# Performance work log

Hardware: AMD Instinct MI355X
Metric: run time of the kernel (lower is better)

Reference implementation:

```python
import jax, jax.numpy as jnp
import numpy as np
import math

B, C, H, W = 8, 64, 256, 256
E, NH = 256, 8
HD = E // NH  # 32


def get_coords(h, w):
    xx, yy = jnp.meshgrid(jnp.arange(h, dtype=jnp.float32), jnp.arange(w, dtype=jnp.float32), indexing='ij')
    return jnp.stack((xx.reshape(-1), yy.reshape(-1)), axis=-1)  # [N, 2]


def setup_inputs() -> dict:
    key = jax.random.key(0)
    ks = jax.random.split(key, 12)
    def xavier(k, shape):
        fan_out, fan_in = shape
        a = math.sqrt(6.0 / (fan_in + fan_out))
        return jax.random.uniform(k, shape, jnp.float32, -a, a)
    x = jax.random.normal(ks[0], (B, C, H, W), jnp.float32)
    z = jax.random.normal(ks[1], (B, C), jnp.float32)
    pos = jax.random.uniform(ks[2], (B, NH, 2), jnp.float32) * (H - 1)
    Wq = xavier(ks[3], (E, C)); bq = jnp.zeros((E,), jnp.float32)
    Wk = xavier(ks[4], (E, C)); bk = jnp.zeros((E,), jnp.float32)
    Wv = xavier(ks[5], (E, C)); bv = jnp.zeros((E,), jnp.float32)
    Wp = xavier(ks[6], (HD, 2)); bp = jax.random.uniform(ks[7], (HD,), jnp.float32, -1.0, 1.0) / math.sqrt(2.0)
    return {"x": x, "z": z, "pos": pos, "Wq": Wq, "bq": bq, "Wk": Wk, "bk": bk,
            "Wv": Wv, "bv": bv, "Wp": Wp, "bp": bp}


def reference(x, z, pos, Wq, bq, Wk, bk, Wv, bv, Wp, bp):
    b, c, h, w = x.shape
    n = h * w
    x_flat = x.reshape(b, c, n).transpose(0, 2, 1)          # [B, N, C]
    pos_grid = get_coords(h, w)                              # [N, 2]
    q = (z @ Wq.T + bq).reshape(b, NH, HD)                   # [B, H, hd]
    k = (x_flat @ Wk.T + bk).reshape(b, n, NH, HD)           # [B, N, H, hd]
    # relative-position modulation of keys
    rel = pos_grid[None, :, None, :] - pos[:, None, :, :]    # [B, N, H, 2]
    qxk = rel @ Wp.T + bp                                    # [B, N, H, hd]
    k = k * qxk
    v = x_flat @ Wv.T + bv                                   # [B, N, E]
    attn_logits = jnp.einsum('bhc,bnhc->bnh', q, k) / math.sqrt(HD)
    attention = jax.nn.softmax(attn_logits, axis=1)          # softmax over N
    pos_out = jnp.einsum('bnh,nx->bhx', attention, pos_grid) # [B, H, 2]
    values = jnp.einsum('bnh,bnc->bhc', attention, v)        # [B, H, E]
    return (values, pos_out)
```

## Files before the change

kernel.cpp:

```cpp
#include <hip/hip_runtime.h>

#define NN    65536
#define NSUB  128
#define NBLK  (NN/NSUB)
#define NTILE 8

typedef short bf16x8 __attribute__((ext_vector_type(8)));
typedef float f32x4v __attribute__((ext_vector_type(4)));
typedef unsigned short ushort_t;
typedef unsigned int uint_t;

#define BUFSZ   36864
#define XLO_OFF 18432
#define SLICE   4608
#define LGSTR   28
#define PSTR    40
#define PST_OFF 1536
#define RED_B   73728
#define SMEM_BYTES 74112

#define WTHI_B  0
#define WTLO_B  32768
#define CJ_B    65536
#define PM_B    66304
#define PL_B    197376
#define PSP_B   328448
#define PSX_B   590592
#define Q_B     8979200
#define QSTR    68

__device__ __forceinline__ uint_t bf16_rne_bits(float f) {
  uint_t u = __float_as_uint(f);
  return (u + 0x7FFFu + ((u >> 16) & 1u)) >> 16;
}
__device__ __forceinline__ uint_t cvt_pk_bf16(float a, float b) {
  uint_t r;
  asm("v_cvt_pk_bf16_f32 %0, %1, %2" : "=v"(r) : "v"(a), "v"(b));
  return r;
}
template <int CTRL, int RMASK = 0xf>
__device__ __forceinline__ float dpp_add(float x) {
  int t = __builtin_amdgcn_update_dpp(0, __float_as_int(x), CTRL, RMASK, 0xf, false);
  return x + __int_as_float(t);
}
template <int CTRL, int RMASK = 0xf>
__device__ __forceinline__ float dpp_maxs(float x) {
  int t = __builtin_amdgcn_update_dpp((int)0xFF800000u, __float_as_int(x), CTRL, RMASK, 0xf, false);
  return fmaxf(x, __int_as_float(t));
}
__device__ __forceinline__ float half_sum(float x) {
  x = dpp_add<0x111>(x); x = dpp_add<0x112>(x); x = dpp_add<0x114>(x);
  x = dpp_add<0x118>(x); x = dpp_add<0x142, 0xA>(x);
  return x;
}
__device__ __forceinline__ float half_max(float x) {
  x = dpp_maxs<0x111>(x); x = dpp_maxs<0x112>(x); x = dpp_maxs<0x114>(x);
  x = dpp_maxs<0x118>(x); x = dpp_maxs<0x142, 0xA>(x);
  return x;
}

__global__ __launch_bounds__(64) void prep_kernel(
    const float* __restrict__ z,  const float* __restrict__ Wq, const float* __restrict__ bq,
    const float* __restrict__ Wk, const float* __restrict__ bk,
    const float* __restrict__ Wp, const float* __restrict__ bp,
    ushort_t* __restrict__ WThi, ushort_t* __restrict__ WTlo, float* __restrict__ Cj)
{
  const int h = blockIdx.x, b = blockIdx.y, t = threadIdx.x;
  __shared__ float q[32];
  if (t < 32) {
    const int e = h*32 + t;
    float a = bq[e];
    const float* zr = z + b*64;
    const float* wr = Wq + e*64;
    #pragma unroll 8
    for (int c = 0; c < 64; ++c) a += zr[c]*wr[c];
    q[t] = a;
  }
  __syncthreads();
  const int c = t;
  float w[3] = {0.f, 0.f, 0.f};
  #pragma unroll 4
  for (int hd = 0; hd < 32; ++hd) {
    const float qk = q[hd] * Wk[(h*32+hd)*64 + c];
    w[0] += qk * bp[hd];
    w[1] += qk * Wp[hd*2+0];
    w[2] += qk * Wp[hd*2+1];
  }
  #pragma unroll
  for (int j = 0; j < 3; ++j) {
    const int coeff = h*3 + j;
    const uint_t hb = bf16_rne_bits(w[j]);
    const float  fh = __uint_as_float(hb << 16);
    const uint_t lb = bf16_rne_bits(w[j] - fh);
    WThi[(b*32 + coeff)*64 + c] = (ushort_t)hb;
    WTlo[(b*32 + coeff)*64 + c] = (ushort_t)lb;
  }
  if (h == 0) {
    #pragma unroll
    for (int r = 0; r < 8; ++r) {
      WThi[(b*32 + 24 + r)*64 + c] = 0;
      WTlo[(b*32 + 24 + r)*64 + c] = 0;
    }
  }
  if (t < 3) {
    float s = 0.f;
    for (int hd = 0; hd < 32; ++hd) {
      const float m = (t == 0) ? bp[hd] : Wp[hd*2 + (t-1)];
      s += q[hd] * m * bk[h*32+hd];
    }
    Cj[b*24 + h*3 + t] = s;
  }
}

__global__ __launch_bounds__(256, 2) void main_kernel(
    const float* __restrict__ x, const float* __restrict__ pos,
    const ushort_t* __restrict__ WThi, const ushort_t* __restrict__ WTlo,
    const float* __restrict__ Cj,
    float* __restrict__ Pm, float* __restrict__ Pl,
    float* __restrict__ Psp, float* __restrict__ Psx)
{
  extern __shared__ char smc[];
  float* red = (float*)(smc + RED_B);
  const int t    = threadIdx.x;
  const int blk0 = blockIdx.x;
  const int b    = blockIdx.y;
  const int w    = t >> 6, lid = t & 63;
  const int c0   = lid & 15, q4 = lid >> 4;
  const int hg   = lid >> 5, pxl = lid & 31;

  bf16x8 bh[2][2], bl[2][2];
  {
    const ushort_t* wtb_h = WThi + b*2048;
    const ushort_t* wtb_l = WTlo + b*2048;
    #pragma unroll
    for (int nt = 0; nt < 2; ++nt)
      #pragma unroll
      for (int ks = 0; ks < 2; ++ks) {
        const int off = (nt*16 + c0)*64 + ks*32 + q4*8;
        bh[nt][ks] = *(const bf16x8*)(wtb_h + off);
        bl[nt][ks] = *(const bf16x8*)(wtb_l + off);
      }
  }

  float cj[12];
  {
    const float* cjp = Cj + b*24 + hg*12;
    #pragma unroll
    for (int k = 0; k < 12; ++k) cj[k] = cjp[k];
  }
  float posx[4], py[4];
  #pragma unroll
  for (int hl = 0; hl < 4; ++hl) {
    const int h = hg*4 + hl;
    posx[hl] = pos[(b*8+h)*2 + 0];
    py[hl]   = pos[(b*8+h)*2 + 1];
  }

  const int qd  = lid & 7;
  const int g   = lid >> 3;
  const int swz = (4*w + (qd >> 1)) & 7;
  const int chnk = (g ^ swz) * 16;
  const float* xg = x + (size_t)b*64*NN + (size_t)g*8*NN
                      + (size_t)blk0*NTILE*NSUB + w*32 + 4*qd;
  f32x4v v[8];
  #pragma unroll
  for (int j = 0; j < 8; ++j) v[j] = *(const f32x4v*)(xg + (size_t)j*NN);

  for (int it = 0; it < NTILE; ++it) {
    const int blk = blk0*NTILE + it;
    char* bufb  = smc + (it & 1)*BUFSZ;
    char* xhiB  = bufb;
    char* xloB  = bufb + XLO_OFF;
    char* slice = xloB + w*SLICE;

    #pragma unroll
    for (int i = 0; i < 4; ++i) {
      uint_t H[4], L[4];
      #pragma unroll
      for (int jp = 0; jp < 4; ++jp) {
        const float f0 = v[2*jp][i], f1 = v[2*jp+1][i];
        const uint_t hpk = cvt_pk_bf16(f0, f1);
        const float h0 = __uint_as_float(hpk << 16);
        const float h1 = __uint_as_float(hpk & 0xFFFF0000u);
        const uint_t l0 = __float_as_uint(f0 - h0);
        const uint_t l1 = __float_as_uint(f1 - h1);
        H[jp] = hpk;
        L[jp] = __builtin_amdgcn_perm(l1, l0, 0x07060302u);
      }
      const int row = w*32 + 4*qd + i;
      *(uint4*)(xhiB + row*144 + chnk) = make_uint4(H[0], H[1], H[2], H[3]);
      *(uint4*)(xloB + row*144 + chnk) = make_uint4(L[0], L[1], L[2], L[3]);
    }

    if (it + 1 < NTILE) {
      xg += NSUB;
      #pragma unroll
      for (int j = 0; j < 8; ++j) v[j] = *(const f32x4v*)(xg + (size_t)j*NN);
    }

    f32x4v acc[2][2];
    #pragma unroll
    for (int mt = 0; mt < 2; ++mt) { acc[mt][0] = (f32x4v)0.f; acc[mt][1] = (f32x4v)0.f; }
    #pragma unroll
    for (int mt = 0; mt < 2; ++mt) {
      const int row  = w*32 + mt*16 + c0;
      const int srow = (4*w + 2*mt + (c0 >> 3)) & 7;
      const int ch0  = (q4 ^ srow) * 16;
      const char* rh = xhiB + row*144;
      const char* rl = xloB + row*144;
      bf16x8 ah0 = *(const bf16x8*)(rh + ch0);
      bf16x8 ah1 = *(const bf16x8*)(rh + (ch0 ^ 64));
      bf16x8 al0 = *(const bf16x8*)(rl + ch0);
      bf16x8 al1 = *(const bf16x8*)(rl + (ch0 ^ 64));
      #pragma unroll
      for (int nt = 0; nt < 2; ++nt) {
        f32x4v a = acc[mt][nt];
        a = __builtin_amdgcn_mfma_f32_16x16x32_bf16(ah0, bh[nt][0], a, 0, 0, 0);
        a = __builtin_amdgcn_mfma_f32_16x16x32_bf16(ah1, bh[nt][1], a, 0, 0, 0);
        a = __builtin_amdgcn_mfma_f32_16x16x32_bf16(ah0, bl[nt][0], a, 0, 0, 0);
        a = __builtin_amdgcn_mfma_f32_16x16x32_bf16(ah1, bl[nt][1], a, 0, 0, 0);
        a = __builtin_amdgcn_mfma_f32_16x16x32_bf16(al0, bh[nt][0], a, 0, 0, 0);
        a = __builtin_amdgcn_mfma_f32_16x16x32_bf16(al1, bh[nt][1], a, 0, 0, 0);
        acc[mt][nt] = a;
      }
    }

    {
      float* lga_w = (float*)slice;
      #pragma unroll
      for (int mt = 0; mt < 2; ++mt)
        #pragma unroll
        for (int r = 0; r < 4; ++r) {
          const int prow = mt*16 + q4*4 + r;
          lga_w[prow*LGSTR + c0] = acc[mt][0][r];
          if (c0 < 8) lga_w[prow*LGSTR + 16 + c0] = acc[mt][1][r];
        }
    }

    float a12[12];
    {
      const float4* ap = (const float4*)((float*)slice + pxl*LGSTR + hg*12);
      #pragma unroll
      for (int r = 0; r < 3; ++r) *(float4*)(a12 + 4*r) = ap[r];
    }
    const float gxf = (float)(blk >> 1);
    const float tf  = (float)(((blk & 1) << 7) + w*32 + pxl);
    float lg[4];
    #pragma unroll
    for (int hl = 0; hl < 4; ++hl) {
      const float a0 = a12[hl*3+0] + cj[hl*3+0];
      const float a1 = a12[hl*3+1] + cj[hl*3+1];
      const float a2 = a12[hl*3+2] + cj[hl*3+2];
      lg[hl] = (a0 + (gxf - posx[hl])*a1 + (tf - py[hl])*a2) * 0.17677669529663687f;
    }

    #pragma unroll
    for (int hl = 0; hl < 4; ++hl) {
      const float m = half_max(lg[hl]);
      if ((lid & 31) == 31) red[w*8 + hg*4 + hl] = m;
    }
    __syncthreads();

    float p[4];
    #pragma unroll
    for (int hl = 0; hl < 4; ++hl) {
      const int h = hg*4 + hl;
      const float M = fmaxf(fmaxf(red[0*8+h], red[1*8+h]), fmaxf(red[2*8+h], red[3*8+h]));
      p[hl] = __expf(lg[hl] - M);
    }

    #pragma unroll
    for (int hl = 0; hl < 4; ++hl) {
      const float sp  = half_sum(p[hl]);
      const float spj = half_sum(p[hl] * tf);
      if ((lid & 31) == 31) {
        red[32 + w*8 + hg*4 + hl] = sp;
        red[64 + w*8 + hg*4 + hl] = spj;
      }
    }
    {
      ushort_t* pls = (ushort_t*)slice;
      #pragma unroll
      for (int hl = 0; hl < 4; ++hl) {
        const int h = hg*4 + hl;
        const uint_t hb = bf16_rne_bits(p[hl]);
        const float  hf = __uint_as_float(hb << 16);
        const uint_t lb = __float_as_uint(p[hl] - hf) >> 16;
        pls[h*PSTR + pxl]     = (ushort_t)hb;
        pls[(h+8)*PSTR + pxl] = (ushort_t)lb;
      }
    }

    {
      const ushort_t* pls = (const ushort_t*)slice;
      const bf16x8 afr = *(const bf16x8*)(pls + c0*PSTR + q4*8);
      const int srow_b = (4*w + q4) & 7;
      float* pst = (float*)(slice + PST_OFF);
      #pragma unroll
      for (int nt = 0; nt < 4; ++nt) {
        const int gch  = nt*2 + (c0 >> 3);
        const char* base = xhiB + (w*32 + q4*8)*144 + ((gch ^ srow_b)*16) + (c0 & 7)*2;
        bf16x8 bfr;
        #pragma unroll
        for (int j = 0; j < 8; ++j) bfr[j] = *(const short*)(base + j*144);
        f32x4v accB = __builtin_amdgcn_mfma_f32_16x16x32_bf16(afr, bfr, (f32x4v)0.f, 0, 0, 0);
        #pragma unroll
        for (int r = 0; r < 4; ++r) {
          const float o = __shfl_xor(accB[r], 32, 64);
          if (q4 < 2) pst[(q4*4 + r)*64 + nt*16 + c0] = accB[r] + o;
        }
      }
    }
    __syncthreads();

    if (t < 8) {
      const int base = (b*NBLK + blk)*8 + t;
      const float M  = fmaxf(fmaxf(red[0*8+t], red[8+t]), fmaxf(red[16+t], red[24+t]));
      const float L  = red[32+t] + red[40+t] + red[48+t] + red[56+t];
      const float SJ = red[64+t] + red[72+t] + red[80+t] + red[88+t];
      Pm[base] = M;
      Pl[base] = L;
      Psp[base*2+0] = gxf * L;
      Psp[base*2+1] = SJ;
    }
    {
      const size_t pb64 = ((size_t)(b*NBLK + blk))*8*64;
      #pragma unroll
      for (int r = 0; r < 2; ++r) {
        const int idx = t + 256*r;
        float s = 0.f;
        #pragma unroll
        for (int w2 = 0; w2 < 4; ++w2)
          s += *(const float*)(xloB + w2*SLICE + PST_OFF + idx*4);
        Psx[pb64 + idx] = s;
      }
    }
  }
}

__global__ __launch_bounds__(256) void reduce1_kernel(
    const float* __restrict__ Pm, const float* __restrict__ Pl,
    const float* __restrict__ Psp, const float* __restrict__ Psx,
    float* __restrict__ Q)
{
  const int g = blockIdx.x, h = blockIdx.y, b = blockIdx.z, t = threadIdx.x;
  __shared__ float al[64];
  __shared__ float mgs;
  __shared__ float sums[3];
  __shared__ float sxl[256];
  const int base = (b*NBLK + g*64)*8 + h;

  float m_t = -1e30f;
  if (t < 64) {
    m_t = Pm[base + t*8];
    float mm = m_t;
    #pragma unroll
    for (int off = 32; off >= 1; off >>= 1) mm = fmaxf(mm, __shfl_xor(mm, off, 64));
    if (t == 0) mgs = mm;
  }
  __syncthreads();
  const float Mg = mgs;
  if (t < 64) {
    const float a = __expf(m_t - Mg);
    al[t] = a;
    float lt = Pl[base + t*8] * a;
    float sx = Psp[(base + t*8)*2 + 0] * a;
    float sy = Psp[(base + t*8)*2 + 1] * a;
    #pragma unroll
    for (int off = 32; off >= 1; off >>= 1) {
      lt += __shfl_xor(lt, off, 64);
      sx += __shfl_xor(sx, off, 64);
      sy += __shfl_xor(sy, off, 64);
    }
    if (t == 0) { sums[0] = lt; sums[1] = sx; sums[2] = sy; }
  }
  __syncthreads();
  {
    const int c = t & 63, g2 = t >> 6;
    float acc = 0.f;
    #pragma unroll
    for (int i = 0; i < 16; ++i) {
      const int k = g2*16 + i;
      acc += al[k] * Psx[(size_t)(base + k*8)*64 + c];
    }
    sxl[g2*64 + c] = acc;
  }
  __syncthreads();
  float* q = Q + ((b*8 + h)*8 + g)*QSTR;
  if (t < 64) q[4+t] = sxl[t] + sxl[64+t] + sxl[128+t] + sxl[192+t];
  if (t == 0) { q[0] = Mg; q[1] = sums[0]; q[2] = sums[1]; q[3] = sums[2]; }
}

__global__ __launch_bounds__(64) void reduce2_kernel(
    const float* __restrict__ Q, const float* __restrict__ Wv, const float* __restrict__ bv,
    float* __restrict__ out)
{
  const int h = blockIdx.x, b = blockIdx.y, t = threadIdx.x;
  __shared__ float qm[8], bl[8], l8[8], sx8[8], sy8[8];
  __shared__ float SXs[64];
  const float* qb = Q + ((b*8 + h)*8)*QSTR;

  if (t < 8) qm[t] = qb[t*QSTR + 0];
  __syncthreads();
  float M = qm[0];
  #pragma unroll
  for (int g = 1; g < 8; ++g) M = fmaxf(M, qm[g]);
  if (t < 8) {
    const float be = __expf(qm[t] - M);
    bl[t]  = be;
    l8[t]  = be * qb[t*QSTR + 1];
    sx8[t] = be * qb[t*QSTR + 2];
    sy8[t] = be * qb[t*QSTR + 3];
  }
  __syncthreads();
  float L = 0.f;
  #pragma unroll
  for (int g = 0; g < 8; ++g) L += l8[g];
  const float invL = 1.0f / L;
  {
    float s = 0.f;
    #pragma unroll
    for (int g = 0; g < 8; ++g) s += bl[g] * qb[g*QSTR + 4 + t];
    SXs[t] = s * invL;
  }
  __syncthreads();

  #pragma unroll
  for (int r = 0; r < 4; ++r) {
    const int e = t + 64*r;
    float v = bv[e];
    const float* wvr = Wv + e*64;
    #pragma unroll 8
    for (int c = 0; c < 64; ++c) v += wvr[c] * SXs[c];
    out[(b*8 + h)*256 + e] = v;
  }
  if (t == 0) {
    float spx = 0.f, spy = 0.f;
    #pragma unroll
    for (int g = 0; g < 8; ++g) { spx += sx8[g]; spy += sy8[g]; }
    out[16384 + (b*8 + h)*2 + 0] = spx * invL;
    out[16384 + (b*8 + h)*2 + 1] = spy * invL;
  }
}

extern "C" void kernel_launch(void* const* d_in, const int* in_sizes, int n_in,
                              void* d_out, int out_size, void* d_ws, size_t ws_size,
                              hipStream_t stream)
{
  const float* x   = (const float*)d_in[0];
  const float* z   = (const float*)d_in[1];
  const float* pos = (const float*)d_in[2];
  const float* Wq  = (const float*)d_in[3];
  const float* bq  = (const float*)d_in[4];
  const float* Wk  = (const float*)d_in[5];
  const float* bk  = (const float*)d_in[6];
  const float* Wv  = (const float*)d_in[7];
  const float* bv  = (const float*)d_in[8];
  const float* Wp  = (const float*)d_in[9];
  const float* bp  = (const float*)d_in[10];
  float* out = (float*)d_out;
  char*  wsb = (char*)d_ws;

  ushort_t* WThi = (ushort_t*)(wsb + WTHI_B);
  ushort_t* WTlo = (ushort_t*)(wsb + WTLO_B);
  float* Cj  = (float*)(wsb + CJ_B);
  float* Pm  = (float*)(wsb + PM_B);
  float* Pl  = (float*)(wsb + PL_B);
  float* Psp = (float*)(wsb + PSP_B);
  float* Psx = (float*)(wsb + PSX_B);
  float* Q   = (float*)(wsb + Q_B);

  (void)hipFuncSetAttribute((const void*)main_kernel,
                            hipFuncAttributeMaxDynamicSharedMemorySize, SMEM_BYTES);

  prep_kernel   <<<dim3(8,8),          64,  0,          stream>>>(z, Wq, bq, Wk, bk, Wp, bp, WThi, WTlo, Cj);
  main_kernel   <<<dim3(NBLK/NTILE,8), 256, SMEM_BYTES, stream>>>(x, pos, WThi, WTlo, Cj, Pm, Pl, Psp, Psx);
  reduce1_kernel<<<dim3(8,8,8),        256, 0,          stream>>>(Pm, Pl, Psp, Psx, Q);
  reduce2_kernel<<<dim3(8,8),          64,  0,          stream>>>(Q, Wv, bv, out);
}
```

Before: 246.2 us.

## Make each wave own its tiles with online softmax, removing block barriers

Each wave now processes its own run of 32-pixel tiles and keeps a running max, sum and weighted-x accumulator in registers, rescaling them online. This removes the per-tile __syncthreads, the shared reduction buffers and the per-tile partial stores to global memory. Shared memory drops to a single buffer, so occupancy can rise (launch bounds go to 4 blocks). Each wave writes one partial record at the end, so the partial layout changes to per-wave granularity, which must still match what reduce1 expects. The added costs are extra exp and shuffle work for the rescaling and higher register pressure.

```diff
diff --git a/kernel.cpp b/kernel.cpp
--- a/kernel.cpp
+++ b/kernel.cpp
@@ -1,23 +1,19 @@
 #include <hip/hip_runtime.h>
 
 #define NN    65536
-#define NSUB  128
-#define NBLK  (NN/NSUB)
-#define NTILE 8
+#define NBLK  512
+#define TPW   4
 
 typedef short bf16x8 __attribute__((ext_vector_type(8)));
 typedef float f32x4v __attribute__((ext_vector_type(4)));
 typedef unsigned short ushort_t;
 typedef unsigned int uint_t;
 
-#define BUFSZ   36864
 #define XLO_OFF 18432
 #define SLICE   4608
 #define LGSTR   28
 #define PSTR    40
-#define PST_OFF 1536
-#define RED_B   73728
-#define SMEM_BYTES 74112
+#define SMEM_BYTES 36864
 
 #define WTHI_B  0
 #define WTLO_B  32768
@@ -57,6 +53,11 @@
   x = dpp_maxs<0x111>(x); x = dpp_maxs<0x112>(x); x = dpp_maxs<0x114>(x);
   x = dpp_maxs<0x118>(x); x = dpp_maxs<0x142, 0xA>(x);
   return x;
+}
+__device__ __forceinline__ float bcast_half(float x, bool hi_half) {
+  const int v0 = __builtin_amdgcn_readlane(__float_as_int(x), 31);
+  const int v1 = __builtin_amdgcn_readlane(__float_as_int(x), 63);
+  return __int_as_float(hi_half ? v1 : v0);
 }
 
 __global__ __launch_bounds__(64) void prep_kernel(
@@ -112,7 +113,7 @@
   }
 }
 
-__global__ __launch_bounds__(256, 2) void main_kernel(
+__global__ __launch_bounds__(256, 4) void main_kernel(
     const float* __restrict__ x, const float* __restrict__ pos,
     const ushort_t* __restrict__ WThi, const ushort_t* __restrict__ WTlo,
     const float* __restrict__ Cj,
@@ -120,13 +121,18 @@
     float* __restrict__ Psp, float* __restrict__ Psx)
 {
   extern __shared__ char smc[];
-  float* red = (float*)(smc + RED_B);
-  const int t    = threadIdx.x;
-  const int blk0 = blockIdx.x;
-  const int b    = blockIdx.y;
-  const int w    = t >> 6, lid = t & 63;
-  const int c0   = lid & 15, q4 = lid >> 4;
-  const int hg   = lid >> 5, pxl = lid & 31;
+  const int t   = threadIdx.x;
+  const int b   = blockIdx.y;
+  const int w   = t >> 6, lid = t & 63;
+  const int c0  = lid & 15, q4 = lid >> 4;
+  const int hg  = lid >> 5, pxl = lid & 31;
+  const bool hihalf = (lid >= 32);
+  const int wave_id = blockIdx.x*4 + w;
+  const int tile0   = wave_id * TPW;
+
+  char* xhiB  = smc;
+  char* xloB  = smc + XLO_OFF;
+  char* slice = xloB + w*SLICE;
 
   bf16x8 bh[2][2], bl[2][2];
   {
@@ -148,31 +154,32 @@
     #pragma unroll
     for (int k = 0; k < 12; ++k) cj[k] = cjp[k];
   }
-  float posx[4], py[4];
+  const float gxf = (float)(wave_id >> 1);
+  float rxh[4], py[4];
   #pragma unroll
   for (int hl = 0; hl < 4; ++hl) {
     const int h = hg*4 + hl;
-    posx[hl] = pos[(b*8+h)*2 + 0];
-    py[hl]   = pos[(b*8+h)*2 + 1];
+    rxh[hl] = gxf - pos[(b*8+h)*2 + 0];
+    py[hl]  = pos[(b*8+h)*2 + 1];
   }
 
   const int qd  = lid & 7;
   const int g   = lid >> 3;
   const int swz = (4*w + (qd >> 1)) & 7;
   const int chnk = (g ^ swz) * 16;
-  const float* xg = x + (size_t)b*64*NN + (size_t)g*8*NN
-                      + (size_t)blk0*NTILE*NSUB + w*32 + 4*qd;
+  const float* xg = x + (size_t)b*64*NN + (size_t)g*8*NN + (size_t)tile0*32 + 4*qd;
   f32x4v v[8];
   #pragma unroll
   for (int j = 0; j < 8; ++j) v[j] = *(const f32x4v*)(xg + (size_t)j*NN);
 
-  for (int it = 0; it < NTILE; ++it) {
-    const int blk = blk0*NTILE + it;
-    char* bufb  = smc + (it & 1)*BUFSZ;
-    char* xhiB  = bufb;
-    char* xloB  = bufb + XLO_OFF;
-    char* slice = xloB + w*SLICE;
-
+  float Mh[4], Lh[4], SJh[4];
+  #pragma unroll
+  for (int hl = 0; hl < 4; ++hl) { Mh[hl] = -1e30f; Lh[hl] = 0.f; SJh[hl] = 0.f; }
+  float sx[16];
+  #pragma unroll
+  for (int i = 0; i < 16; ++i) sx[i] = 0.f;
+
+  for (int it = 0; it < TPW; ++it) {
     #pragma unroll
     for (int i = 0; i < 4; ++i) {
       uint_t H[4], L[4];
@@ -192,8 +199,8 @@
       *(uint4*)(xloB + row*144 + chnk) = make_uint4(L[0], L[1], L[2], L[3]);
     }
 
-    if (it + 1 < NTILE) {
-      xg += NSUB;
+    if (it + 1 < TPW) {
+      xg += 32;
       #pragma unroll
       for (int j = 0; j < 8; ++j) v[j] = *(const f32x4v*)(xg + (size_t)j*NN);
     }
@@ -243,41 +250,33 @@
       #pragma unroll
       for (int r = 0; r < 3; ++r) *(float4*)(a12 + 4*r) = ap[r];
     }
-    const float gxf = (float)(blk >> 1);
-    const float tf  = (float)(((blk & 1) << 7) + w*32 + pxl);
+    const float tf = (float)((((tile0 + it) & 7) << 5) + pxl);
     float lg[4];
     #pragma unroll
     for (int hl = 0; hl < 4; ++hl) {
       const float a0 = a12[hl*3+0] + cj[hl*3+0];
       const float a1 = a12[hl*3+1] + cj[hl*3+1];
       const float a2 = a12[hl*3+2] + cj[hl*3+2];
-      lg[hl] = (a0 + (gxf - posx[hl])*a1 + (tf - py[hl])*a2) * 0.17677669529663687f;
-    }
-
+      lg[hl] = (a0 + rxh[hl]*a1 + (tf - py[hl])*a2) * 0.17677669529663687f;
+    }
+
+    float rs[4], p[4];
     #pragma unroll
     for (int hl = 0; hl < 4; ++hl) {
-      const float m = half_max(lg[hl]);
-      if ((lid & 31) == 31) red[w*8 + hg*4 + hl] = m;
-    }
-    __syncthreads();
-
-    float p[4];
-    #pragma unroll
-    for (int hl = 0; hl < 4; ++hl) {
-      const int h = hg*4 + hl;
-      const float M = fmaxf(fmaxf(red[0*8+h], red[1*8+h]), fmaxf(red[2*8+h], red[3*8+h]));
-      p[hl] = __expf(lg[hl] - M);
-    }
-
+      const float mt_ = bcast_half(half_max(lg[hl]), hihalf);
+      const float Mn  = fmaxf(Mh[hl], mt_);
+      rs[hl] = __expf(Mh[hl] - Mn);
+      p[hl]  = __expf(lg[hl] - Mn);
+      Mh[hl] = Mn;
+    }
     #pragma unroll
     for (int hl = 0; hl < 4; ++hl) {
       const float sp  = half_sum(p[hl]);
       const float spj = half_sum(p[hl] * tf);
-      if ((lid & 31) == 31) {
-        red[32 + w*8 + hg*4 + hl] = sp;
-        red[64 + w*8 + hg*4 + hl] = spj;
-      }
-    }
+      Lh[hl]  = Lh[hl]*rs[hl]  + sp;
+      SJh[hl] = SJh[hl]*rs[hl] + spj;
+    }
+
     {
       ushort_t* pls = (ushort_t*)slice;
       #pragma unroll
@@ -291,11 +290,17 @@
       }
     }
 
+    float rsu[4];
+    #pragma unroll
+    for (int r = 0; r < 4; ++r) {
+      const float ro = __shfl_xor(rs[r], 32, 64);
+      rsu[r] = (q4 & 1) ? ro : rs[r];
+    }
+
     {
       const ushort_t* pls = (const ushort_t*)slice;
       const bf16x8 afr = *(const bf16x8*)(pls + c0*PSTR + q4*8);
       const int srow_b = (4*w + q4) & 7;
-      float* pst = (float*)(slice + PST_OFF);
       #pragma unroll
       for (int nt = 0; nt < 4; ++nt) {
         const int gch  = nt*2 + (c0 >> 3);
@@ -307,34 +312,30 @@
         #pragma unroll
         for (int r = 0; r < 4; ++r) {
           const float o = __shfl_xor(accB[r], 32, 64);
-          if (q4 < 2) pst[(q4*4 + r)*64 + nt*16 + c0] = accB[r] + o;
+          sx[nt*4 + r] = sx[nt*4 + r]*rsu[r] + (accB[r] + o);
         }
       }
     }
-    __syncthreads();
-
-    if (t < 8) {
-      const int base = (b*NBLK + blk)*8 + t;
-      const float M  = fmaxf(fmaxf(red[0*8+t], red[8+t]), fmaxf(red[16+t], red[24+t]));
-      const float L  = red[32+t] + red[40+t] + red[48+t] + red[56+t];
-      const float SJ = red[64+t] + red[72+t] + red[80+t] + red[88+t];
-      Pm[base] = M;
-      Pl[base] = L;
-      Psp[base*2+0] = gxf * L;
-      Psp[base*2+1] = SJ;
-    }
-    {
-      const size_t pb64 = ((size_t)(b*NBLK + blk))*8*64;
-      #pragma unroll
-      for (int r = 0; r < 2; ++r) {
-        const int idx = t + 256*r;
-        float s = 0.f;
-        #pragma unroll
-        for (int w2 = 0; w2 < 4; ++w2)
-          s += *(const float*)(xloB + w2*SLICE + PST_OFF + idx*4);
-        Psx[pb64 + idx] = s;
-      }
-    }
+  }
+
+  const int pbase = (b*NBLK + wave_id)*8;
+  if ((lid & 31) == 31) {
+    #pragma unroll
+    for (int hl = 0; hl < 4; ++hl) {
+      const int h = hg*4 + hl;
+      Pm[pbase + h] = Mh[hl];
+      Pl[pbase + h] = Lh[hl];
+      Psp[(pbase + h)*2 + 0] = gxf * Lh[hl];
+      Psp[(pbase + h)*2 + 1] = SJh[hl];
+    }
+  }
+  if (q4 < 2) {
+    const size_t pb64 = (size_t)pbase * 64;
+    #pragma unroll
+    for (int nt = 0; nt < 4; ++nt)
+      #pragma unroll
+      for (int r = 0; r < 4; ++r)
+        Psx[pb64 + (q4*4 + r)*64 + nt*16 + c0] = sx[nt*4 + r];
   }
 }
 
@@ -364,15 +365,15 @@
     const float a = __expf(m_t - Mg);
     al[t] = a;
     float lt = Pl[base + t*8] * a;
-    float sx = Psp[(base + t*8)*2 + 0] * a;
-    float sy = Psp[(base + t*8)*2 + 1] * a;
+    float sxv = Psp[(base + t*8)*2 + 0] * a;
+    float syv = Psp[(base + t*8)*2 + 1] * a;
     #pragma unroll
     for (int off = 32; off >= 1; off >>= 1) {
-      lt += __shfl_xor(lt, off, 64);
-      sx += __shfl_xor(sx, off, 64);
-      sy += __shfl_xor(sy, off, 64);
-    }
-    if (t == 0) { sums[0] = lt; sums[1] = sx; sums[2] = sy; }
+      lt  += __shfl_xor(lt, off, 64);
+      sxv += __shfl_xor(sxv, off, 64);
+      syv += __shfl_xor(syv, off, 64);
+    }
+    if (t == 0) { sums[0] = lt; sums[1] = sxv; sums[2] = syv; }
   }
   __syncthreads();
   {
@@ -470,11 +471,8 @@
   float* Psx = (float*)(wsb + PSX_B);
   float* Q   = (float*)(wsb + Q_B);
 
-  (void)hipFuncSetAttribute((const void*)main_kernel,
-                            hipFuncAttributeMaxDynamicSharedMemorySize, SMEM_BYTES);
-
-  prep_kernel   <<<dim3(8,8),          64,  0,          stream>>>(z, Wq, bq, Wk, bk, Wp, bp, WThi, WTlo, Cj);
-  main_kernel   <<<dim3(NBLK/NTILE,8), 256, SMEM_BYTES, stream>>>(x, pos, WThi, WTlo, Cj, Pm, Pl, Psp, Psx);
-  reduce1_kernel<<<dim3(8,8,8),        256, 0,          stream>>>(Pm, Pl, Psp, Psx, Q);
-  reduce2_kernel<<<dim3(8,8),          64,  0,          stream>>>(Q, Wv, bv, out);
-}
+  prep_kernel   <<<dim3(8,8),   64,  0,          stream>>>(z, Wq, bq, Wk, bk, Wp, bp, WThi, WTlo, Cj);
+  main_kernel   <<<dim3(128,8), 256, SMEM_BYTES, stream>>>(x, pos, WThi, WTlo, Cj, Pm, Pl, Psp, Psx);
+  reduce1_kernel<<<dim3(8,8,8), 256, 0,          stream>>>(Pm, Pl, Psp, Psx, Q);
+  reduce2_kernel<<<dim3(8,8),   64,  0,          stream>>>(Q, Wv, bv, out);
+}
```

After: 277.3 us. 1.13x slower.
